# Kernel optimization log

Measured on AMD Instinct MI355X. Metric: run time of the kernel, lower is better.

Reference implementation:

```python
import jax, jax.numpy as jnp
import numpy as np

NB_HEADS = 12


def setup_inputs() -> dict:
    key = jax.random.key(0)
    ks = jax.random.split(key, 6)
    B, S, D, H = 4, 1024, 768, NB_HEADS
    x = jax.random.normal(ks[0], (B, S, D), dtype=jnp.float32)
    Wqkv = jax.random.normal(ks[1], (D, 3 * D), dtype=jnp.float32) * 0.02
    bqkv = jnp.zeros((3 * D,), dtype=jnp.float32)
    Wl = jax.random.normal(ks[2], (H, H), dtype=jnp.float32) * 0.3
    bl = jnp.zeros((H,), dtype=jnp.float32)
    Ww = jax.random.normal(ks[3], (H, H), dtype=jnp.float32) * 0.3
    bw = jnp.zeros((H,), dtype=jnp.float32)
    Wproj = jax.random.normal(ks[4], (D, D), dtype=jnp.float32) * 0.02
    bproj = jnp.zeros((D,), dtype=jnp.float32)
    return {"x": x, "Wqkv": Wqkv, "bqkv": bqkv, "Wl": Wl, "bl": bl,
            "Ww": Ww, "bw": bw, "Wproj": Wproj, "bproj": bproj}


def reference(x, Wqkv, bqkv, Wl, bl, Ww, bw, Wproj, bproj):
    B, S, D = x.shape
    H = NB_HEADS
    dh = D // H
    scale = dh ** (-0.5)
    # qkv projection: [B,S,3D] -> [3,B,H,S,dh]
    qkv = (x @ Wqkv + bqkv).reshape(B, S, 3, H, dh).transpose(2, 0, 3, 1, 4)
    q, k, v = qkv[0] * scale, qkv[1], qkv[2]
    # raw attention logits [B,H,S,S]
    attn = jnp.einsum('bhqd,bhkd->bhqk', q, k)
    # pre-softmax talking-heads mix across head dim (Dense over heads)
    attn = jnp.einsum('bhqk,hg->bgqk', attn, Wl) + bl[None, :, None, None]
    attn = jax.nn.softmax(attn, axis=-1)
    # post-softmax talking-heads mix
    attn = jnp.einsum('bhqk,hg->bgqk', attn, Ww) + bw[None, :, None, None]
    # attention-weighted values -> [B,S,D]
    out = jnp.einsum('bhqk,bhkd->bqhd', attn, v).reshape(B, S, D)
    return out @ Wproj + bproj
```

## Files before the change

kernel.cpp:

```cpp
#include <hip/hip_runtime.h>
#include <cstdint>

#define BB 4
#define SS 1024
#define DD 768
#define HH 12
#define DH 64

typedef unsigned short u16;
typedef unsigned int   u32;
typedef __attribute__((ext_vector_type(8))) short bf16x8;
typedef __attribute__((ext_vector_type(4))) float f32x4;

__device__ __forceinline__ u16 f2bf(float f) {
    u32 u = __float_as_uint(f);
    u += 0x7fffu + ((u >> 16) & 1u);
    return (u16)(u >> 16);
}
__device__ __forceinline__ float b2f(u32 lo16) {
    return __uint_as_float(lo16 << 16);
}
__device__ __forceinline__ u32 pack2(float a, float b) {
    return (u32)f2bf(a) | ((u32)f2bf(b) << 16);
}

#define ASYNC16(gp, lp) __builtin_amdgcn_global_load_lds( \
    (const __attribute__((address_space(1))) void*)(gp),  \
    (__attribute__((address_space(3))) void*)(lp), 16, 0, 0)

template<int BM_, int BN_, class Epi>
__device__ __forceinline__ void mfma_gemm(
    const u16* __restrict__ A, const u16* __restrict__ B,
    int K, int lda, int ldb, int m0, int n0, const Epi& epi)
{
    constexpr int MI = BM_ / 32;
    constexpr int NJ = BN_ / 32;
    __shared__ u16 Alds[BM_ * 32];
    __shared__ u16 Blds[BN_ * 32];

    const int tid  = threadIdx.x;
    const int wave = tid >> 6;
    const int lane = tid & 63;
    const int wr = wave >> 1, wc = wave & 1;

    const int ar = lane >> 2;
    const int ac = (lane & 3) * 8;

    f32x4 acc[MI][NJ] = {};

    for (int k0 = 0; k0 < K; k0 += 32) {
        __syncthreads();
#pragma unroll
        for (int j = 0; j < BM_ / 64; ++j) {
            const int rb = wave * (BM_ / 4) + j * 16;
            ASYNC16(A + (size_t)(m0 + rb + ar) * lda + k0 + ac, &Alds[rb * 32]);
        }
#pragma unroll
        for (int j = 0; j < BN_ / 64; ++j) {
            const int rb = wave * (BN_ / 4) + j * 16;
            ASYNC16(B + (size_t)(n0 + rb + ar) * ldb + k0 + ac, &Blds[rb * 32]);
        }
        __syncthreads();

        bf16x8 af[MI], bfr[NJ];
#pragma unroll
        for (int mi = 0; mi < MI; ++mi)
            af[mi] = *(const bf16x8*)&Alds[(wr * (BM_ / 2) + mi * 16 + (lane & 15)) * 32 + (lane >> 4) * 8];
#pragma unroll
        for (int nj = 0; nj < NJ; ++nj)
            bfr[nj] = *(const bf16x8*)&Blds[(wc * (BN_ / 2) + nj * 16 + (lane & 15)) * 32 + (lane >> 4) * 8];
#pragma unroll
        for (int mi = 0; mi < MI; ++mi)
#pragma unroll
            for (int nj = 0; nj < NJ; ++nj)
                acc[mi][nj] = __builtin_amdgcn_mfma_f32_16x16x32_bf16(
                    af[mi], bfr[nj], acc[mi][nj], 0, 0, 0);
    }

#pragma unroll
    for (int mi = 0; mi < MI; ++mi)
#pragma unroll
        for (int nj = 0; nj < NJ; ++nj)
#pragma unroll
            for (int r = 0; r < 4; ++r)
                epi(m0 + wr * (BM_ / 2) + mi * 16 + (lane >> 4) * 4 + r,
                    n0 + wc * (BN_ / 2) + nj * 16 + (lane & 15),
                    acc[mi][nj][r]);
}


__global__ __launch_bounds__(256) void qkv_gemm_kernel(
    const u16* __restrict__ xb, const u16* __restrict__ Wt,
    const float* __restrict__ bias,
    u16* __restrict__ qb, u16* __restrict__ kb, u16* __restrict__ vt)
{
    struct Epi {
        const float* bias; u16 *qb, *kb, *vt;
        __device__ void operator()(int m, int n, float v) const {
            const float val = v + bias[n];
            const int c = n / DD;
            const int w = n - c * DD, h = w >> 6, d = w & 63;
            const int b = m >> 10, s = m & 1023;
            if (c == 0)
                qb[(((size_t)(b * HH + h) << 10) + s) * DH + d] = f2bf(val * 0.125f);
            else if (c == 1)
                kb[(((size_t)(b * HH + h) << 10) + s) * DH + d] = f2bf(val);
            else
                vt[((size_t)(b * HH + h) * DH + d) * SS + s] = f2bf(val);
        }
    } epi{bias, qb, kb, vt};
    mfma_gemm<128, 128>(xb, Wt, DD, DD, DD, blockIdx.y * 128, blockIdx.x * 128, epi);
}

__global__ __launch_bounds__(256) void qk_gemm_kernel(
    const u16* __restrict__ qb, const u16* __restrict__ kb,
    u16* __restrict__ attn, int bh0)
{
    const int bhL = blockIdx.z;
    const int bh = bh0 + bhL;
    const u16* A = qb + (size_t)bh * SS * DH;
    const u16* B = kb + (size_t)bh * SS * DH;
    u16* C = attn + (size_t)bhL * SS * SS;
    struct Epi {
        u16* C;
        __device__ void operator()(int m, int n, float v) const {
            C[(size_t)m * SS + n] = f2bf(v);
        }
    } epi{C};
    mfma_gemm<128, 128>(A, B, DH, DH, DH, blockIdx.y * 128, blockIdx.x * 128, epi);
}

__global__ __launch_bounds__(256) void pv_gemm_kernel(
    const u16* __restrict__ attn2, const u16* __restrict__ vt,
    u16* __restrict__ ctx, int bh0)
{
    const int bhL = blockIdx.z;
    const int bh = bh0 + bhL;
    const int b = bh / HH, h = bh % HH;
    const u16* A = attn2 + (size_t)bhL * SS * SS;
    const u16* B = vt + (size_t)bh * DH * SS;
    u16* C = ctx + (size_t)b * SS * DD + h * DH;
    struct Epi {
        u16* C;
        __device__ void operator()(int m, int n, float v) const {
            C[(size_t)m * DD + n] = f2bf(v);
        }
    } epi{C};
    mfma_gemm<128, 64>(A, B, SS, SS, SS, blockIdx.y * 128, 0, epi);
}

__global__ __launch_bounds__(256) void proj_gemm_kernel(
    const u16* __restrict__ ctx, const u16* __restrict__ Wt,
    const float* __restrict__ bias, float* __restrict__ out)
{
    struct Epi {
        float* out; const float* bias;
        __device__ void operator()(int m, int n, float v) const {
            out[(size_t)m * DD + n] = v + bias[n];
        }
    } epi{out, bias};
    mfma_gemm<128, 64>(ctx, Wt, DD, DD, DD, blockIdx.y * 128, blockIdx.x * 64, epi);
}

__global__ __launch_bounds__(256) void mix_softmax_kernel(
    const u16* __restrict__ attn, u16* __restrict__ attn2,
    const float* __restrict__ Wl, const float* __restrict__ bl,
    const float* __restrict__ Ww, const float* __restrict__ bw)
{
    __shared__ float redS[4][HH];

    const int tid  = threadIdx.x;
    const int wave = tid >> 6;
    const int lane = tid & 63;
    const int bL = blockIdx.x >> 10;
    const int qi = blockIdx.x & (SS - 1);
    const size_t base = ((size_t)bL * HH * SS + qi) * SS + tid * 4;

    float vin[HH][4];
#pragma unroll
    for (int h = 0; h < HH; ++h) {
        const uint2 u = *(const uint2*)&attn[base + (size_t)h * SS * SS];
        vin[h][0] = b2f(u.x & 0xffff); vin[h][1] = b2f(u.x >> 16);
        vin[h][2] = b2f(u.y & 0xffff); vin[h][3] = b2f(u.y >> 16);
    }

    float e[HH][4];
    float psum[HH];
#pragma unroll
    for (int g = 0; g < HH; ++g) {
        const float bg = bl[g];
        float s0 = bg, s1 = bg, s2 = bg, s3 = bg;
#pragma unroll
        for (int h = 0; h < HH; ++h) {
            const float w = Wl[h * HH + g];
            s0 += vin[h][0] * w; s1 += vin[h][1] * w;
            s2 += vin[h][2] * w; s3 += vin[h][3] * w;
        }
        s0 = __expf(s0); s1 = __expf(s1); s2 = __expf(s2); s3 = __expf(s3);
        e[g][0] = s0; e[g][1] = s1; e[g][2] = s2; e[g][3] = s3;
        psum[g] = (s0 + s1) + (s2 + s3);
    }

#pragma unroll
    for (int g = 0; g < HH; ++g)
#pragma unroll
        for (int off = 32; off; off >>= 1)
            psum[g] += __shfl_xor(psum[g], off);
    if (lane == 0)
#pragma unroll
        for (int g = 0; g < HH; ++g) redS[wave][g] = psum[g];
    __syncthreads();

#pragma unroll
    for (int h = 0; h < HH; ++h) {
        const float inv = 1.0f /
            ((redS[0][h] + redS[1][h]) + (redS[2][h] + redS[3][h]));
        e[h][0] *= inv; e[h][1] *= inv; e[h][2] *= inv; e[h][3] *= inv;
    }

#pragma unroll
    for (int g = 0; g < HH; ++g) {
        const float bg = bw[g];
        float s0 = bg, s1 = bg, s2 = bg, s3 = bg;
#pragma unroll
        for (int h = 0; h < HH; ++h) {
            const float w = Ww[h * HH + g];
            s0 += e[h][0] * w; s1 += e[h][1] * w;
            s2 += e[h][2] * w; s3 += e[h][3] * w;
        }
        uint2 p;
        p.x = pack2(s0, s1); p.y = pack2(s2, s3);
        *(uint2*)&attn2[base + (size_t)g * SS * SS] = p;
    }
}


__global__ __launch_bounds__(256) void cvt_bf16_kernel(
    const float* __restrict__ in, u16* __restrict__ out, int n8)
{
    const int i = blockIdx.x * 256 + threadIdx.x;
    if (i >= n8) return;
    const float4 a = ((const float4*)in)[i * 2];
    const float4 b = ((const float4*)in)[i * 2 + 1];
    uint4 p;
    p.x = pack2(a.x, a.y); p.y = pack2(a.z, a.w);
    p.z = pack2(b.x, b.y); p.w = pack2(b.z, b.w);
    ((uint4*)out)[i] = p;
}

__global__ __launch_bounds__(256) void cvt_transpose_kernel(
    const float* __restrict__ in, u16* __restrict__ out, int R, int C)
{
    __shared__ float t[32][33];
    const int c0 = blockIdx.x * 32, r0 = blockIdx.y * 32;
    const int tr = threadIdx.x >> 3;
    const int tc = (threadIdx.x & 7) * 4;
    const float4 v = *(const float4*)&in[(size_t)(r0 + tr) * C + c0 + tc];
    t[tc + 0][tr] = v.x; t[tc + 1][tr] = v.y;
    t[tc + 2][tr] = v.z; t[tc + 3][tr] = v.w;
    __syncthreads();
    uint2 p;
    p.x = pack2(t[tr][tc + 0], t[tr][tc + 1]);
    p.y = pack2(t[tr][tc + 2], t[tr][tc + 3]);
    *(uint2*)&out[(size_t)(c0 + tr) * R + r0 + tc] = p;
}

extern "C" void kernel_launch(void* const* d_in, const int* in_sizes, int n_in,
                              void* d_out, int out_size, void* d_ws, size_t ws_size,
                              hipStream_t stream)
{
    const float* x     = (const float*)d_in[0];
    const float* Wqkv  = (const float*)d_in[1];
    const float* bqkv  = (const float*)d_in[2];
    const float* Wl    = (const float*)d_in[3];
    const float* bl    = (const float*)d_in[4];
    const float* Ww    = (const float*)d_in[5];
    const float* bw    = (const float*)d_in[6];
    const float* Wproj = (const float*)d_in[7];
    const float* bproj = (const float*)d_in[8];
    float* out = (float*)d_out;

    const size_t N_XB  = (size_t)BB * SS * DD;
    const size_t N_QB  = (size_t)BB * HH * SS * DH;
    const size_t N_WT  = (size_t)DD * 3 * DD;
    const size_t N_WP  = (size_t)DD * DD;
    const size_t N_AT1 = (size_t)HH * SS * SS;

    u16* xb  = (u16*)d_ws;
    u16* qb  = xb  + N_XB;
    u16* kb  = qb  + N_QB;
    u16* vt  = kb  + N_QB;
    u16* ctx = vt  + N_QB;
    u16* Wqkv_t = ctx + N_XB;
    u16* Wproj_t = Wqkv_t + N_WT;
    u16* attn = Wproj_t + N_WP;

    const size_t fixed_bytes = (size_t)(N_XB * 2 + N_QB * 3 + N_WT + N_WP) * 2;
    int b_per = BB;
    while (b_per > 1 &&
           fixed_bytes + (size_t)b_per * N_AT1 * 2 * 2 > ws_size)
        b_per >>= 1;
    const int n_iter = BB / b_per;
    u16* attn2 = attn + (size_t)b_per * N_AT1;

    const dim3 blk(256);

    cvt_bf16_kernel<<<dim3((N_XB / 8 + 255) / 256), blk, 0, stream>>>(x, xb, (int)(N_XB / 8));
    cvt_transpose_kernel<<<dim3(3 * DD / 32, DD / 32), blk, 0, stream>>>(Wqkv, Wqkv_t, DD, 3 * DD);
    cvt_transpose_kernel<<<dim3(DD / 32, DD / 32), blk, 0, stream>>>(Wproj, Wproj_t, DD, DD);

    qkv_gemm_kernel<<<dim3(3 * DD / 128, BB * SS / 128), blk, 0, stream>>>(
        xb, Wqkv_t, bqkv, qb, kb, vt);

    for (int it = 0; it < n_iter; ++it) {
        const int bh0 = it * b_per * HH;
        qk_gemm_kernel<<<dim3(SS / 128, SS / 128, b_per * HH), blk, 0, stream>>>(
            qb, kb, attn, bh0);
        mix_softmax_kernel<<<dim3(b_per * SS), blk, 0, stream>>>(
            attn, attn2, Wl, bl, Ww, bw);
        pv_gemm_kernel<<<dim3(1, SS / 128, b_per * HH), blk, 0, stream>>>(
            attn2, vt, ctx, bh0);
    }

    proj_gemm_kernel<<<dim3(DD / 64, BB * SS / 128), blk, 0, stream>>>(
        ctx, Wproj_t, bproj, out);
}
```

Measured before the change: 268.3 us.

## Double GEMM K-step to 64 and stage mix-softmax rows through LDS

The shared MFMA GEMM now loads 64-wide K slices per iteration, so it runs two MFMA sub-steps per barrier pair, halving loop and sync overhead. The mix-softmax kernel now brings all 12 head rows into LDS with async global-to-LDS loads. It then stores the exponentials as bf16 in LDS, which cuts register pressure from keeping e[12][4] live across the reduction. The trade-offs are more LDS per block, an extra bf16 rounding of the exponentials before normalisation, and one more barrier.

```diff
diff --git a/kernel.cpp b/kernel.cpp
--- a/kernel.cpp
+++ b/kernel.cpp
@@ -35,46 +35,51 @@
 {
     constexpr int MI = BM_ / 32;
     constexpr int NJ = BN_ / 32;
-    __shared__ u16 Alds[BM_ * 32];
-    __shared__ u16 Blds[BN_ * 32];
+    __shared__ u16 Alds[BM_ * 64];
+    __shared__ u16 Blds[BN_ * 64];
 
     const int tid  = threadIdx.x;
     const int wave = tid >> 6;
     const int lane = tid & 63;
     const int wr = wave >> 1, wc = wave & 1;
 
-    const int ar = lane >> 2;
-    const int ac = (lane & 3) * 8;
+    const int ar = lane >> 3;
+    const int ac = (lane & 7) * 8;
 
     f32x4 acc[MI][NJ] = {};
 
-    for (int k0 = 0; k0 < K; k0 += 32) {
+    for (int k0 = 0; k0 < K; k0 += 64) {
         __syncthreads();
 #pragma unroll
-        for (int j = 0; j < BM_ / 64; ++j) {
-            const int rb = wave * (BM_ / 4) + j * 16;
-            ASYNC16(A + (size_t)(m0 + rb + ar) * lda + k0 + ac, &Alds[rb * 32]);
-        }
-#pragma unroll
-        for (int j = 0; j < BN_ / 64; ++j) {
-            const int rb = wave * (BN_ / 4) + j * 16;
-            ASYNC16(B + (size_t)(n0 + rb + ar) * ldb + k0 + ac, &Blds[rb * 32]);
+        for (int j = 0; j < BM_ / 32; ++j) {
+            const int rb = wave * (BM_ / 4) + j * 8;
+            ASYNC16(A + (size_t)(m0 + rb + ar) * lda + k0 + ac, &Alds[rb * 64]);
+        }
+#pragma unroll
+        for (int j = 0; j < BN_ / 32; ++j) {
+            const int rb = wave * (BN_ / 4) + j * 8;
+            ASYNC16(B + (size_t)(n0 + rb + ar) * ldb + k0 + ac, &Blds[rb * 64]);
         }
         __syncthreads();
 
-        bf16x8 af[MI], bfr[NJ];
-#pragma unroll
-        for (int mi = 0; mi < MI; ++mi)
-            af[mi] = *(const bf16x8*)&Alds[(wr * (BM_ / 2) + mi * 16 + (lane & 15)) * 32 + (lane >> 4) * 8];
-#pragma unroll
-        for (int nj = 0; nj < NJ; ++nj)
-            bfr[nj] = *(const bf16x8*)&Blds[(wc * (BN_ / 2) + nj * 16 + (lane & 15)) * 32 + (lane >> 4) * 8];
-#pragma unroll
-        for (int mi = 0; mi < MI; ++mi)
+#pragma unroll
+        for (int ki = 0; ki < 2; ++ki) {
+            bf16x8 af[MI], bfr[NJ];
+#pragma unroll
+            for (int mi = 0; mi < MI; ++mi)
+                af[mi] = *(const bf16x8*)&Alds[(wr * (BM_ / 2) + mi * 16 + (lane & 15)) * 64
+                                               + ki * 32 + (lane >> 4) * 8];
 #pragma unroll
             for (int nj = 0; nj < NJ; ++nj)
-                acc[mi][nj] = __builtin_amdgcn_mfma_f32_16x16x32_bf16(
-                    af[mi], bfr[nj], acc[mi][nj], 0, 0, 0);
+                bfr[nj] = *(const bf16x8*)&Blds[(wc * (BN_ / 2) + nj * 16 + (lane & 15)) * 64
+                                                + ki * 32 + (lane >> 4) * 8];
+#pragma unroll
+            for (int mi = 0; mi < MI; ++mi)
+#pragma unroll
+                for (int nj = 0; nj < NJ; ++nj)
+                    acc[mi][nj] = __builtin_amdgcn_mfma_f32_16x16x32_bf16(
+                        af[mi], bfr[nj], acc[mi][nj], 0, 0, 0);
+        }
     }
 
 #pragma unroll
@@ -167,29 +172,41 @@
     const float* __restrict__ Wl, const float* __restrict__ bl,
     const float* __restrict__ Ww, const float* __restrict__ bw)
 {
+    __shared__ u16 buf[HH][SS];
     __shared__ float redS[4][HH];
+    __shared__ float invS[HH];
 
     const int tid  = threadIdx.x;
     const int wave = tid >> 6;
     const int lane = tid & 63;
     const int bL = blockIdx.x >> 10;
     const int qi = blockIdx.x & (SS - 1);
-    const size_t base = ((size_t)bL * HH * SS + qi) * SS + tid * 4;
+    const size_t grow = ((size_t)bL * HH * SS + qi) * SS;
+
+#pragma unroll
+    for (int j = 0; j < 6; ++j) {
+        const int c = wave * 6 + j;
+        const int h = c >> 1, hf = c & 1;
+        ASYNC16(attn + grow + (size_t)h * SS * SS + hf * 512 + lane * 8,
+                &buf[h][hf * 512]);
+    }
+    __syncthreads();
+
+    const int kc = tid * 4;
+    const size_t gbase = grow + kc;
 
     float vin[HH][4];
 #pragma unroll
     for (int h = 0; h < HH; ++h) {
-        const uint2 u = *(const uint2*)&attn[base + (size_t)h * SS * SS];
+        const uint2 u = *(const uint2*)&buf[h][kc];
         vin[h][0] = b2f(u.x & 0xffff); vin[h][1] = b2f(u.x >> 16);
         vin[h][2] = b2f(u.y & 0xffff); vin[h][3] = b2f(u.y >> 16);
     }
 
-    float e[HH][4];
     float psum[HH];
 #pragma unroll
     for (int g = 0; g < HH; ++g) {
-        const float bg = bl[g];
-        float s0 = bg, s1 = bg, s2 = bg, s3 = bg;
+        float s0 = bl[g], s1 = s0, s2 = s0, s3 = s0;
 #pragma unroll
         for (int h = 0; h < HH; ++h) {
             const float w = Wl[h * HH + g];
@@ -197,31 +214,36 @@
             s2 += vin[h][2] * w; s3 += vin[h][3] * w;
         }
         s0 = __expf(s0); s1 = __expf(s1); s2 = __expf(s2); s3 = __expf(s3);
-        e[g][0] = s0; e[g][1] = s1; e[g][2] = s2; e[g][3] = s3;
         psum[g] = (s0 + s1) + (s2 + s3);
-    }
-
-#pragma unroll
-    for (int g = 0; g < HH; ++g)
-#pragma unroll
-        for (int off = 32; off; off >>= 1)
-            psum[g] += __shfl_xor(psum[g], off);
-    if (lane == 0)
-#pragma unroll
-        for (int g = 0; g < HH; ++g) redS[wave][g] = psum[g];
+        uint2 p;
+        p.x = pack2(s0, s1); p.y = pack2(s2, s3);
+        *(uint2*)&buf[g][kc] = p;
+    }
+
+#pragma unroll
+    for (int g = 0; g < HH; ++g) {
+        float t = psum[g];
+#pragma unroll
+        for (int off = 32; off; off >>= 1) t += __shfl_xor(t, off);
+        if (lane == 0) redS[wave][g] = t;
+    }
     __syncthreads();
-
+    if (tid < HH)
+        invS[tid] = 1.0f / ((redS[0][tid] + redS[1][tid]) +
+                            (redS[2][tid] + redS[3][tid]));
+    __syncthreads();
+
+    float e[HH][4];
 #pragma unroll
     for (int h = 0; h < HH; ++h) {
-        const float inv = 1.0f /
-            ((redS[0][h] + redS[1][h]) + (redS[2][h] + redS[3][h]));
-        e[h][0] *= inv; e[h][1] *= inv; e[h][2] *= inv; e[h][3] *= inv;
-    }
-
+        const uint2 u = *(const uint2*)&buf[h][kc];
+        const float inv = invS[h];
+        e[h][0] = b2f(u.x & 0xffff) * inv; e[h][1] = b2f(u.x >> 16) * inv;
+        e[h][2] = b2f(u.y & 0xffff) * inv; e[h][3] = b2f(u.y >> 16) * inv;
+    }
 #pragma unroll
     for (int g = 0; g < HH; ++g) {
-        const float bg = bw[g];
-        float s0 = bg, s1 = bg, s2 = bg, s3 = bg;
+        float s0 = bw[g], s1 = s0, s2 = s0, s3 = s0;
 #pragma unroll
         for (int h = 0; h < HH; ++h) {
             const float w = Ww[h * HH + g];
@@ -230,7 +252,7 @@
         }
         uint2 p;
         p.x = pack2(s0, s1); p.y = pack2(s2, s3);
-        *(uint2*)&attn2[base + (size_t)g * SS * SS] = p;
+        *(uint2*)&attn2[gbase + (size_t)g * SS * SS] = p;
     }
 }
 
```

Result: slower. 288.2 us (+7.4%).
